# Optimization experiments

Hardware: AMD Instinct MI355X
Metric: run time of the kernel (lower is better)

Reference implementation:

```python
import jax, jax.numpy as jnp
import numpy as np

EPS = 1e-5

def layernorm(x, g, b):
    mu = jnp.mean(x, axis=-1, keepdims=True)
    var = jnp.var(x, axis=-1, keepdims=True)
    return (x - mu) * jax.lax.rsqrt(var + EPS) * g + b

DIM = 1024; CTX = 1024; HEADS = 12; DHEAD = 64; INNER = HEADS * DHEAD
B = 4; F = 2048; J = 1024

def setup_inputs() -> dict:
    key = jax.random.key(0)
    ks = jax.random.split(key, 8)
    s = lambda d: 1.0 / np.sqrt(d)
    return {
        "x": jax.random.normal(ks[0], (B, F, DIM), jnp.float32),
        "tab_x": jax.random.normal(ks[1], (B, J, CTX), jnp.float32),
        "tab_g": jnp.ones((CTX,), jnp.float32), "tab_b": jnp.zeros((CTX,), jnp.float32),
        "vid_g": jnp.ones((DIM,), jnp.float32), "vid_b": jnp.zeros((DIM,), jnp.float32),
        "Wq": jax.random.normal(ks[2], (DIM, INNER), jnp.float32) * s(DIM),
        "Wk": jax.random.normal(ks[3], (CTX, INNER), jnp.float32) * s(CTX),
        "Wv": jax.random.normal(ks[4], (CTX, INNER), jnp.float32) * s(CTX),
        "q_g": jnp.ones((INNER,), jnp.float32), "q_b": jnp.zeros((INNER,), jnp.float32),
        "k_g": jnp.ones((INNER,), jnp.float32), "k_b": jnp.zeros((INNER,), jnp.float32),
        "Wo": jax.random.normal(ks[5], (INNER, DIM), jnp.float32) * s(INNER),
        "bo": jnp.zeros((DIM,), jnp.float32),
    }

def reference(x, tab_x, tab_g, tab_b, vid_g, vid_b, Wq, Wk, Wv, q_g, q_b, k_g, k_b, Wo, bo):
    scale = DHEAD ** -0.5
    kv_in = layernorm(tab_x, tab_g, tab_b)                      # [b,j,ctx]
    q = layernorm(layernorm(x, vid_g, vid_b) @ Wq, q_g, q_b)    # [b,f,inner]
    k = layernorm(kv_in @ Wk, k_g, k_b)                         # [b,j,inner]
    v = kv_in @ Wv                                              # [b,j,inner]
    split = lambda t: t.reshape(t.shape[0], t.shape[1], HEADS, DHEAD).transpose(0, 2, 1, 3)
    q, k, v = split(q) * scale, split(k), split(v)              # [b,h,*,d]
    sim = jnp.einsum('bhid,bhjd->bhij', q, k)
    attn = jax.nn.softmax(sim, axis=-1)
    out = jnp.einsum('bhij,bhjd->bhid', attn, v)                # [b,h,f,d]
    out = out.transpose(0, 2, 1, 3).reshape(x.shape[0], x.shape[1], INNER)
    return out @ Wo + bo
```

## Files before the change

### kernel.cpp

```cpp
#include <hip/hip_runtime.h>

typedef unsigned short u16;
typedef float  f32x4   __attribute__((ext_vector_type(4)));
typedef float  f32x16  __attribute__((ext_vector_type(16)));
typedef __bf16 bf16x8  __attribute__((ext_vector_type(8)));
typedef u16    u16x4   __attribute__((ext_vector_type(4)));

#define DEV __device__ __forceinline__

DEV u16 f2bf(float f) {
  union { float f; unsigned u; } x; x.f = f;
  unsigned r = x.u + 0x7fffu + ((x.u >> 16) & 1u);
  return (u16)(r >> 16);
}
DEV float bf2f(u16 b) { union { unsigned u; float f; } c; c.u = (unsigned)b << 16; return c.f; }

DEV unsigned cvtpk(float lo, float hi) {
  unsigned r;
  asm("v_cvt_pk_bf16_f32 %0, %1, %2" : "=v"(r) : "v"(lo), "v"(hi));
  return r;
}

DEV f32x4 mfma16(bf16x8 a, bf16x8 b, f32x4 c) {
  return __builtin_amdgcn_mfma_f32_16x16x32_bf16(a, b, c, 0, 0, 0);
}
DEV f32x16 mfma32(bf16x8 a, bf16x8 b, f32x16 c) {
  return __builtin_amdgcn_mfma_f32_32x32x16_bf16(a, b, c, 0, 0, 0);
}

DEV void gload16(const void* g, void* l) {
  __builtin_amdgcn_global_load_lds(
      (__attribute__((address_space(1))) void*)g,
      (__attribute__((address_space(3))) void*)l, 16, 0, 0);
}

template<typename LOADER>
DEV void ln_body(LOADER load, const float* __restrict__ g, const float* __restrict__ bta,
                 u16* __restrict__ yrow, int C, float outscale, float* red)
{
  const int tid = threadIdx.x;
  const int n4 = C >> 2;
  f32x4 v = {0.f, 0.f, 0.f, 0.f};
  if (tid < n4) v = load(tid);
  float s1 = v[0] + v[1] + v[2] + v[3];
  float s2 = v[0]*v[0] + v[1]*v[1] + v[2]*v[2] + v[3]*v[3];
#pragma unroll
  for (int o = 32; o > 0; o >>= 1) {
    s1 += __shfl_xor(s1, o, 64);
    s2 += __shfl_xor(s2, o, 64);
  }
  const int lane = tid & 63, wv = tid >> 6;
  if (lane == 0) { red[wv] = s1; red[4 + wv] = s2; }
  __syncthreads();
  s1 = red[0] + red[1] + red[2] + red[3];
  s2 = red[4] + red[5] + red[6] + red[7];
  const float mu = s1 / C;
  const float rs = rsqrtf(s2 / C - mu * mu + 1e-5f);
  if (tid < n4) {
    f32x4 gg = *(const f32x4*)(g + 4 * tid);
    f32x4 bb = *(const f32x4*)(bta + 4 * tid);
    u16x4 o4;
#pragma unroll
    for (int j = 0; j < 4; ++j)
      o4[j] = f2bf(((v[j] - mu) * rs * gg[j] + bb[j]) * outscale);
    *(u16x4*)(yrow + 4 * tid) = o4;
  }
}

__global__ __launch_bounds__(256)
void prep(const float* __restrict__ Wq, const float* __restrict__ Wk,
          const float* __restrict__ Wv, const float* __restrict__ Wo,
          u16* __restrict__ WqT, u16* __restrict__ WkvT, u16* __restrict__ WoT,
          const float* __restrict__ tabx, const float* __restrict__ tab_g,
          const float* __restrict__ tab_b,
          const float* __restrict__ x, const float* __restrict__ vid_g,
          const float* __restrict__ vid_b,
          u16* __restrict__ kvn, u16* __restrict__ xn)
{
  __shared__ float t[32][33];
  __shared__ float red[8];
  const int bid = blockIdx.x;
  const int tid = threadIdx.x;
  if (bid < 3840) {
    const float* src; u16* dst; int K, N, k0, n0;
    if (bid < 3072) {
      const int w = bid / 768, r = bid % 768;
      src = (w == 0) ? Wq : (w == 1) ? Wk : Wv;
      dst = (w == 0) ? WqT : (w == 1) ? WkvT : WkvT + (size_t)768 * 1024;
      K = 1024; N = 768; k0 = (r % 32) * 32; n0 = (r / 32) * 32;
    } else {
      const int r = bid - 3072;
      src = Wo; dst = WoT;
      K = 768; N = 1024; k0 = (r % 24) * 32; n0 = (r / 24) * 32;
    }
    const int tx = tid & 31, ty = tid >> 5;
#pragma unroll
    for (int i = ty; i < 32; i += 8)
      t[i][tx] = src[(size_t)(k0 + i) * N + n0 + tx];
    __syncthreads();
#pragma unroll
    for (int i = ty; i < 32; i += 8)
      dst[(size_t)(n0 + i) * K + k0 + tx] = f2bf(t[tx][i]);
  } else {
    const int r = bid - 3840;
    const float* xr; const float *g, *bb; u16* y;
    if (r < 4096) { xr = tabx + (size_t)r * 1024; g = tab_g; bb = tab_b;
                    y = kvn + (size_t)r * 1024; }
    else { const int rr = r - 4096; xr = x + (size_t)rr * 1024; g = vid_g;
           bb = vid_b; y = xn + (size_t)rr * 1024; }
    ln_body([&](int i) { return *(const f32x4*)(xr + 4 * i); }, g, bb, y, 1024, 1.0f, red);
  }
}

__global__ __launch_bounds__(256)
void gemm_qkv(const u16* __restrict__ xn, const u16* __restrict__ kvn,
              const u16* __restrict__ WqT, const u16* __restrict__ WkvT,
              u16* __restrict__ q_pre, u16* __restrict__ k_pre, u16* __restrict__ vb)
{
  __shared__ __align__(16) u16 As[2][64 * 64];
  __shared__ __align__(16) u16 Bs[2][128 * 64];
  const int bid = blockIdx.x;
  const int tid  = threadIdx.x;
  const int lane = tid & 63;
  const int wave = tid >> 6;
  const bool isq = bid >= 768;
  const u16* A; const u16* Bt; int bm, bn;
  if (!isq) { A = kvn;  Bt = WkvT; bm = (bid & 63) * 64;  bn = (bid >> 6) * 128; }
  else { const int r = bid - 768; A = xn; Bt = WqT; bm = (r & 127) * 64; bn = (r >> 7) * 128; }
  const int wm = (wave >> 1) * 32;
  const int wn = (wave & 1) * 64;
  const int fr = lane & 15;
  const int fk = (lane >> 4) * 8;

  f32x4 acc[2][4] = {};
  const char* gA0 = (const char*)(A  + (size_t)bm * 1024);
  const char* gB0 = (const char*)(Bt + (size_t)bn * 1024);
  const size_t rowpitch = 2048;

  auto stage = [&](int buf, int k0) {
#pragma unroll
    for (int c = 0; c < 2; ++c) {
      const int off = tid * 16 + c * 4096;
      gload16(gA0 + (size_t)(off >> 7) * rowpitch + 2 * k0 + (off & 127),
              (char*)&As[buf][0] + wave * 1024 + c * 4096);
    }
#pragma unroll
    for (int c = 0; c < 4; ++c) {
      const int off = tid * 16 + c * 4096;
      gload16(gB0 + (size_t)(off >> 7) * rowpitch + 2 * k0 + (off & 127),
              (char*)&Bs[buf][0] + wave * 1024 + c * 4096);
    }
  };

  stage(0, 0);
  __syncthreads();
  int cur = 0;
  for (int t = 0; t < 16; ++t) {
    if (t + 1 < 16) stage(cur ^ 1, (t + 1) * 64);
    bf16x8 af[2][2], bg[4][2];
#pragma unroll
    for (int m = 0; m < 2; ++m)
#pragma unroll
      for (int kk = 0; kk < 2; ++kk)
        af[m][kk] = *(const bf16x8*)&As[cur][(wm + m * 16 + fr) * 64 + kk * 32 + fk];
#pragma unroll
    for (int n = 0; n < 4; ++n)
#pragma unroll
      for (int kk = 0; kk < 2; ++kk)
        bg[n][kk] = *(const bf16x8*)&Bs[cur][(wn + n * 16 + fr) * 64 + kk * 32 + fk];
#pragma unroll
    for (int kk = 0; kk < 2; ++kk)
#pragma unroll
      for (int m = 0; m < 2; ++m)
#pragma unroll
        for (int n = 0; n < 4; ++n)
          acc[m][n] = mfma16(af[m][kk], bg[n][kk], acc[m][n]);
    if (t + 1 < 16) __syncthreads();
    cur ^= 1;
  }

  const int orow0 = bm + wm + 4 * (lane >> 4);
  const int ocol0 = bn + wn + fr;
#pragma unroll
  for (int m = 0; m < 2; ++m)
#pragma unroll
    for (int n = 0; n < 4; ++n)
#pragma unroll
      for (int r = 0; r < 4; ++r) {
        const int row = orow0 + m * 16 + r;
        const int col = ocol0 + n * 16;
        const u16 v = f2bf(acc[m][n][r]);
        if (isq) q_pre[(size_t)row * 768 + col] = v;
        else if (bn < 768) k_pre[(size_t)row * 768 + col] = v;
        else               vb[(size_t)row * 768 + (col - 768)] = v;
      }
}

__global__ __launch_bounds__(256)
void ln_tv(const u16* __restrict__ k_pre, const float* __restrict__ k_g,
           const float* __restrict__ k_b, u16* __restrict__ kb,
           const u16* __restrict__ q_pre, const float* __restrict__ q_g,
           const float* __restrict__ q_b, u16* __restrict__ qb,
           const u16* __restrict__ vb, u16* __restrict__ vT)
{
  __shared__ u16 t[64][65];
  __shared__ float red[8];
  const int bid = blockIdx.x;
  const int tid = threadIdx.x;
  if (bid < 12288) {
    const bool isk = bid < 4096;
    const int row = isk ? bid : bid - 4096;
    const u16* xr = (isk ? k_pre : q_pre) + (size_t)row * 768;
    u16* y = (isk ? kb : qb) + (size_t)row * 768;
    const float sc = isk ? 1.0f : 0.125f * 1.44269504089f;
    ln_body([&](int i) {
      const u16x4 raw = *(const u16x4*)(xr + 4 * i);
      f32x4 v; 
#pragma unroll
      for (int j = 0; j < 4; ++j) v[j] = bf2f(raw[j]);
      return v;
    }, isk ? k_g : q_g, isk ? k_b : q_b, y, 768, sc, red);
  } else {
    const int r2 = bid - 12288;
    const int bh = r2 % 48, b = bh / 12, h = bh - b * 12;
    const int j0 = (r2 / 48) * 64;
    const int tx = tid & 63, ty = tid >> 6;
#pragma unroll
    for (int i = ty; i < 64; i += 4)
      t[i][tx] = vb[(size_t)(b * 1024 + j0 + i) * 768 + h * 64 + tx];
    __syncthreads();
#pragma unroll
    for (int i = ty; i < 64; i += 4)
      vT[((size_t)bh * 64 + i) * 1024 + j0 + tx] = t[tx][i];
  }
}

__global__ __launch_bounds__(256, 3)
void attn4(const u16* __restrict__ q, const u16* __restrict__ k,
           const u16* __restrict__ vT, u16* __restrict__ att)
{
  __shared__ __align__(16) u16 Ks[2][64 * 64];
  __shared__ __align__(16) u16 Vs[2][64 * 64];
  __shared__ __align__(16) u16 osm[4][32][72];

  const int bh = blockIdx.x;
  const int b = bh / 12, h = bh - b * 12;
  const int tid = threadIdx.x, lane = tid & 63, wave = tid >> 6;
  const int lq  = lane & 31;
  const int hi5 = lane >> 5;
  const int qrow = blockIdx.y * 128 + wave * 32 + lq;

  const u16* qp = q + (size_t)(b * 2048 + qrow) * 768 + h * 64 + hi5 * 8;
  bf16x8 qf[4];
#pragma unroll
  for (int ds = 0; ds < 4; ++ds) qf[ds] = *(const bf16x8*)(qp + ds * 16);

  f32x16 ot0 = {}, ot1 = {};
  float m = -1e30f, l = 0.f;

  const char* kg = (const char*)k + (size_t)(b * 1024) * 1536 + h * 128;
  const char* vg = (const char*)vT + (size_t)bh * 64 * 2048;
  const int rsw0 = (lq & 7) << 4;

  auto stage = [&](int buf, int j0) {
#pragma unroll
    for (int c = 0; c < 2; ++c) {
      const int o   = tid * 16 + c * 4096;
      const int row = o >> 7;
      const int scol = (o & 127) ^ ((row & 7) << 4);
      gload16(kg + (size_t)(j0 + row) * 1536 + scol,
              (char*)&Ks[buf][0] + wave * 1024 + c * 4096);
      gload16(vg + (size_t)row * 2048 + j0 * 2 + scol,
              (char*)&Vs[buf][0] + wave * 1024 + c * 4096);
    }
  };

  stage(0, 0);
  __syncthreads();
  int cur = 0;
  for (int t = 0; t < 16; ++t) {
    const int j0 = t * 64;
    if (t + 1 < 16) stage(cur ^ 1, j0 + 64);
    f32x16 st0 = {}, st1 = {};
    __builtin_amdgcn_s_setprio(1);
#pragma unroll
    for (int ds = 0; ds < 4; ++ds) {
      const int cb = ds * 32 + hi5 * 16;
      const bf16x8 k0 = *(const bf16x8*)((const char*)&Ks[cur][0] + lq * 128 + (cb ^ rsw0));
      const bf16x8 k1 = *(const bf16x8*)((const char*)&Ks[cur][0] + (lq + 32) * 128 + (cb ^ rsw0));
      st0 = mfma32(k0, qf[ds], st0);
      st1 = mfma32(k1, qf[ds], st1);
    }
    __builtin_amdgcn_s_setprio(0);
    float ta0 = fmaxf(st0[0], st1[0]), ta1 = fmaxf(st0[1], st1[1]);
    float ta2 = fmaxf(st0[2], st1[2]), ta3 = fmaxf(st0[3], st1[3]);
#pragma unroll
    for (int r = 4; r < 16; r += 4) {
      ta0 = fmaxf(fmaxf(st0[r],     st1[r]),     ta0);
      ta1 = fmaxf(fmaxf(st0[r + 1], st1[r + 1]), ta1);
      ta2 = fmaxf(fmaxf(st0[r + 2], st1[r + 2]), ta2);
      ta3 = fmaxf(fmaxf(st0[r + 3], st1[r + 3]), ta3);
    }
    float tmax = fmaxf(fmaxf(fmaxf(ta0, ta1), ta2), ta3);
    tmax = fmaxf(tmax, __shfl_xor(tmax, 32, 64));
    if (!__all(tmax - m <= 11.5416f)) {
      const float mn = fmaxf(m, tmax);
      const float sc = exp2f(m - mn);
      l *= sc;
#pragma unroll
      for (int r = 0; r < 16; ++r) { ot0[r] *= sc; ot1[r] *= sc; }
      m = mn;
    }
    float sa0 = 0.f, sa1 = 0.f, sa2 = 0.f, sa3 = 0.f;
#pragma unroll
    for (int r = 0; r < 16; r += 4) {
      float p0 = exp2f(st0[r]     - m); st0[r]     = p0; sa0 += p0;
      float p1 = exp2f(st0[r + 1] - m); st0[r + 1] = p1; sa1 += p1;
      float p2 = exp2f(st0[r + 2] - m); st0[r + 2] = p2; sa2 += p2;
      float p3 = exp2f(st0[r + 3] - m); st0[r + 3] = p3; sa3 += p3;
    }
#pragma unroll
    for (int r = 0; r < 16; r += 4) {
      float p0 = exp2f(st1[r]     - m); st1[r]     = p0; sa0 += p0;
      float p1 = exp2f(st1[r + 1] - m); st1[r + 1] = p1; sa1 += p1;
      float p2 = exp2f(st1[r + 2] - m); st1[r + 2] = p2; sa2 += p2;
      float p3 = exp2f(st1[r + 3] - m); st1[r + 3] = p3; sa3 += p3;
    }
    float ts = (sa0 + sa1) + (sa2 + sa3);
    ts += __shfl_xor(ts, 32, 64);
    l += ts;
    __builtin_amdgcn_s_setprio(1);
#pragma unroll
    for (int s4 = 0; s4 < 4; ++s4) {
      const int u = (s4 & 1) * 8;
      float a0, a1, a2, a3, b0, b1, b2, b3;
      if (s4 < 2) {
        a0 = st0[u]; a1 = st0[u + 1]; a2 = st0[u + 2]; a3 = st0[u + 3];
        b0 = st0[u + 4]; b1 = st0[u + 5]; b2 = st0[u + 6]; b3 = st0[u + 7];
      } else {
        a0 = st1[u]; a1 = st1[u + 1]; a2 = st1[u + 2]; a3 = st1[u + 3];
        b0 = st1[u + 4]; b1 = st1[u + 5]; b2 = st1[u + 6]; b3 = st1[u + 7];
      }
      const unsigned L0 = cvtpk(a0, a1), L1 = cvtpk(a2, a3);
      const unsigned H0 = cvtpk(b0, b1), H1 = cvtpk(b2, b3);
      const auto w02 = __builtin_amdgcn_permlane32_swap(L0, H0, false, false);
      const auto w13 = __builtin_amdgcn_permlane32_swap(L1, H1, false, false);
      union BU { unsigned w[4]; bf16x8 v; } pu;
      pu.w[0] = w02[0]; pu.w[1] = w13[0]; pu.w[2] = w02[1]; pu.w[3] = w13[1];
      const int cb = s4 * 32 + hi5 * 16;
      const bf16x8 v0 = *(const bf16x8*)((const char*)&Vs[cur][0] + lq * 128 + (cb ^ rsw0));
      const bf16x8 v1 = *(const bf16x8*)((const char*)&Vs[cur][0] + (lq + 32) * 128 + (cb ^ rsw0));
      ot0 = mfma32(v0, pu.v, ot0);
      ot1 = mfma32(v1, pu.v, ot1);
    }
    __builtin_amdgcn_s_setprio(0);
    if (t + 1 < 16) __syncthreads();
    cur ^= 1;
  }
  const float inv = 1.0f / l;
#pragma unroll
  for (int r = 0; r < 16; ++r) {
    const int d0 = (r & 3) + 8 * (r >> 2) + 4 * hi5;
    osm[wave][lq][d0]      = f2bf(ot0[r] * inv);
    osm[wave][lq][32 + d0] = f2bf(ot1[r] * inv);
  }
  __syncthreads();
  const int col = (lane & 7) * 8;
#pragma unroll
  for (int pass = 0; pass < 4; ++pass) {
    const int row = pass * 8 + (lane >> 3);
    const bf16x8 vv = *(const bf16x8*)&osm[wave][row][col];
    const int qg = blockIdx.y * 128 + wave * 32 + row;
    *(bf16x8*)(att + (size_t)(b * 2048 + qg) * 768 + h * 64 + col) = vv;
  }
}

__global__ __launch_bounds__(256)
void gemm_o(const u16* __restrict__ A, const u16* __restrict__ Bt,
            float* __restrict__ Cp, const float* __restrict__ bias)
{
  __shared__ __align__(16) u16 As[2][64 * 64];
  __shared__ __align__(16) u16 Bs[2][128 * 64];
  const int tid  = threadIdx.x;
  const int lane = tid & 63;
  const int wave = tid >> 6;
  const int bm = blockIdx.x * 64;
  const int bn = blockIdx.y * 128;
  const int wm = (wave >> 1) * 32;
  const int wn = (wave & 1) * 64;
  const int fr = lane & 15;
  const int fk = (lane >> 4) * 8;

  f32x4 acc[2][4] = {};
  const char* gA0 = (const char*)(A  + (size_t)bm * 768);
  const char* gB0 = (const char*)(Bt + (size_t)bn * 768);
  const size_t rowpitch = 1536;

  auto stage = [&](int buf, int k0) {
#pragma unroll
    for (int c = 0; c < 2; ++c) {
      const int off = tid * 16 + c * 4096;
      gload16(gA0 + (size_t)(off >> 7) * rowpitch + 2 * k0 + (off & 127),
              (char*)&As[buf][0] + wave * 1024 + c * 4096);
    }
#pragma unroll
    for (int c = 0; c < 4; ++c) {
      const int off = tid * 16 + c * 4096;
      gload16(gB0 + (size_t)(off >> 7) * rowpitch + 2 * k0 + (off & 127),
              (char*)&Bs[buf][0] + wave * 1024 + c * 4096);
    }
  };

  stage(0, 0);
  __syncthreads();
  int cur = 0;
  for (int t = 0; t < 12; ++t) {
    if (t + 1 < 12) stage(cur ^ 1, (t + 1) * 64);
    bf16x8 af[2][2], bg[4][2];
#pragma unroll
    for (int m = 0; m < 2; ++m)
#pragma unroll
      for (int kk = 0; kk < 2; ++kk)
        af[m][kk] = *(const bf16x8*)&As[cur][(wm + m * 16 + fr) * 64 + kk * 32 + fk];
#pragma unroll
    for (int n = 0; n < 4; ++n)
#pragma unroll
      for (int kk = 0; kk < 2; ++kk)
        bg[n][kk] = *(const bf16x8*)&Bs[cur][(wn + n * 16 + fr) * 64 + kk * 32 + fk];
#pragma unroll
    for (int kk = 0; kk < 2; ++kk)
#pragma unroll
      for (int m = 0; m < 2; ++m)
#pragma unroll
        for (int n = 0; n < 4; ++n)
          acc[m][n] = mfma16(af[m][kk], bg[n][kk], acc[m][n]);
    if (t + 1 < 12) __syncthreads();
    cur ^= 1;
  }

  const int orow0 = bm + wm + 4 * (lane >> 4);
  const int ocol0 = bn + wn + fr;
#pragma unroll
  for (int m = 0; m < 2; ++m)
#pragma unroll
    for (int n = 0; n < 4; ++n)
#pragma unroll
      for (int r = 0; r < 4; ++r) {
        const int row = orow0 + m * 16 + r;
        const int col = ocol0 + n * 16;
        Cp[(size_t)row * 1024 + col] = acc[m][n][r] + bias[col];
      }
}

extern "C" void kernel_launch(void* const* d_in, const int* in_sizes, int n_in,
                              void* d_out, int out_size, void* d_ws, size_t ws_size,
                              hipStream_t stream)
{
  const float* x     = (const float*)d_in[0];
  const float* tabx  = (const float*)d_in[1];
  const float* tab_g = (const float*)d_in[2];
  const float* tab_b = (const float*)d_in[3];
  const float* vid_g = (const float*)d_in[4];
  const float* vid_b = (const float*)d_in[5];
  const float* Wq    = (const float*)d_in[6];
  const float* Wk    = (const float*)d_in[7];
  const float* Wv    = (const float*)d_in[8];
  const float* q_g   = (const float*)d_in[9];
  const float* q_b   = (const float*)d_in[10];
  const float* k_g   = (const float*)d_in[11];
  const float* k_b   = (const float*)d_in[12];
  const float* Wo    = (const float*)d_in[13];
  const float* bo    = (const float*)d_in[14];

  char* ws = (char*)d_ws;
  const size_t O_WQT  = 0;
  const size_t O_WKVT = O_WQT  + (size_t)768 * 1024 * 2;
  const size_t O_WOT  = O_WKVT + (size_t)1536 * 1024 * 2;
  const size_t O_XN   = O_WOT  + (size_t)1024 * 768 * 2;
  const size_t O_KVN  = O_XN   + (size_t)8192 * 1024 * 2;
  const size_t O_QPRE = O_KVN  + (size_t)4096 * 1024 * 2;
  const size_t O_KPRE = O_QPRE + (size_t)8192 * 768 * 2;
  const size_t O_QB   = O_KPRE + (size_t)4096 * 768 * 2;
  const size_t O_KB   = O_QB   + (size_t)8192 * 768 * 2;
  const size_t O_VB   = O_KB   + (size_t)4096 * 768 * 2;
  const size_t O_VT   = O_VB   + (size_t)4096 * 768 * 2;
  const size_t O_ATT  = O_QPRE;

  u16*   WqT   = (u16*)(ws + O_WQT);
  u16*   WkvT  = (u16*)(ws + O_WKVT);
  u16*   WoT   = (u16*)(ws + O_WOT);
  u16*   xn    = (u16*)(ws + O_XN);
  u16*   kvn   = (u16*)(ws + O_KVN);
  u16*   q_pre = (u16*)(ws + O_QPRE);
  u16*   k_pre = (u16*)(ws + O_KPRE);
  u16*   qb    = (u16*)(ws + O_QB);
  u16*   kb    = (u16*)(ws + O_KB);
  u16*   vb    = (u16*)(ws + O_VB);
  u16*   vT    = (u16*)(ws + O_VT);
  u16*   attb  = (u16*)(ws + O_ATT);

  prep<<<16128, 256, 0, stream>>>(Wq, Wk, Wv, Wo, WqT, WkvT, WoT,
                                  tabx, tab_g, tab_b, x, vid_g, vid_b, kvn, xn);
  gemm_qkv<<<1536, 256, 0, stream>>>(xn, kvn, WqT, WkvT, q_pre, k_pre, vb);
  ln_tv<<<13056, 256, 0, stream>>>(k_pre, k_g, k_b, kb, q_pre, q_g, q_b, qb, vb, vT);
  attn4<<<dim3(48, 16), 256, 0, stream>>>(qb, kb, vT, attb);
  gemm_o<<<dim3(128, 8), 256, 0, stream>>>(attb, WoT, (float*)d_out, bo);
}
```

Before: 156.9 us.

## Write V transposed from QKV GEMM and split attention keys across wave groups

```diff
diff --git a/kernel.cpp b/kernel.cpp
--- a/kernel.cpp
+++ b/kernel.cpp
@@ -115,7 +115,7 @@
 __global__ __launch_bounds__(256)
 void gemm_qkv(const u16* __restrict__ xn, const u16* __restrict__ kvn,
               const u16* __restrict__ WqT, const u16* __restrict__ WkvT,
-              u16* __restrict__ q_pre, u16* __restrict__ k_pre, u16* __restrict__ vb)
+              u16* __restrict__ q_pre, u16* __restrict__ k_pre, u16* __restrict__ vT)
 {
   __shared__ __align__(16) u16 As[2][64 * 64];
   __shared__ __align__(16) u16 Bs[2][128 * 64];
@@ -184,71 +184,62 @@
 #pragma unroll
   for (int m = 0; m < 2; ++m)
 #pragma unroll
-    for (int n = 0; n < 4; ++n)
-#pragma unroll
-      for (int r = 0; r < 4; ++r) {
-        const int row = orow0 + m * 16 + r;
-        const int col = ocol0 + n * 16;
-        const u16 v = f2bf(acc[m][n][r]);
-        if (isq) q_pre[(size_t)row * 768 + col] = v;
-        else if (bn < 768) k_pre[(size_t)row * 768 + col] = v;
-        else               vb[(size_t)row * 768 + (col - 768)] = v;
+    for (int n = 0; n < 4; ++n) {
+      const int row0 = orow0 + m * 16;
+      const int col  = ocol0 + n * 16;
+      if (isq) {
+#pragma unroll
+        for (int r = 0; r < 4; ++r)
+          q_pre[(size_t)(row0 + r) * 768 + col] = f2bf(acc[m][n][r]);
+      } else if (bn < 768) {
+#pragma unroll
+        for (int r = 0; r < 4; ++r)
+          k_pre[(size_t)(row0 + r) * 768 + col] = f2bf(acc[m][n][r]);
+      } else {
+        const int c2 = col - 768, hh = c2 >> 6, dd = c2 & 63;
+        const int bb2 = row0 >> 10, jj = row0 & 1023;
+        u16x4 o4;
+#pragma unroll
+        for (int r = 0; r < 4; ++r) o4[r] = f2bf(acc[m][n][r]);
+        *(u16x4*)(vT + ((size_t)(bb2 * 12 + hh) * 64 + dd) * 1024 + jj) = o4;
       }
+    }
 }
 
 __global__ __launch_bounds__(256)
-void ln_tv(const u16* __restrict__ k_pre, const float* __restrict__ k_g,
+void ln_qk(const u16* __restrict__ k_pre, const float* __restrict__ k_g,
            const float* __restrict__ k_b, u16* __restrict__ kb,
            const u16* __restrict__ q_pre, const float* __restrict__ q_g,
-           const float* __restrict__ q_b, u16* __restrict__ qb,
-           const u16* __restrict__ vb, u16* __restrict__ vT)
-{
-  __shared__ u16 t[64][65];
+           const float* __restrict__ q_b, u16* __restrict__ qb)
+{
   __shared__ float red[8];
   const int bid = blockIdx.x;
-  const int tid = threadIdx.x;
-  if (bid < 12288) {
-    const bool isk = bid < 4096;
-    const int row = isk ? bid : bid - 4096;
-    const u16* xr = (isk ? k_pre : q_pre) + (size_t)row * 768;
-    u16* y = (isk ? kb : qb) + (size_t)row * 768;
-    const float sc = isk ? 1.0f : 0.125f * 1.44269504089f;
-    ln_body([&](int i) {
-      const u16x4 raw = *(const u16x4*)(xr + 4 * i);
-      f32x4 v; 
-#pragma unroll
-      for (int j = 0; j < 4; ++j) v[j] = bf2f(raw[j]);
-      return v;
-    }, isk ? k_g : q_g, isk ? k_b : q_b, y, 768, sc, red);
-  } else {
-    const int r2 = bid - 12288;
-    const int bh = r2 % 48, b = bh / 12, h = bh - b * 12;
-    const int j0 = (r2 / 48) * 64;
-    const int tx = tid & 63, ty = tid >> 6;
-#pragma unroll
-    for (int i = ty; i < 64; i += 4)
-      t[i][tx] = vb[(size_t)(b * 1024 + j0 + i) * 768 + h * 64 + tx];
-    __syncthreads();
-#pragma unroll
-    for (int i = ty; i < 64; i += 4)
-      vT[((size_t)bh * 64 + i) * 1024 + j0 + tx] = t[tx][i];
-  }
-}
-
-__global__ __launch_bounds__(256, 3)
-void attn4(const u16* __restrict__ q, const u16* __restrict__ k,
+  const bool isk = bid < 4096;
+  const int row = isk ? bid : bid - 4096;
+  const u16* xr = (isk ? k_pre : q_pre) + (size_t)row * 768;
+  u16* y = (isk ? kb : qb) + (size_t)row * 768;
+  const float sc = isk ? 1.0f : 0.125f * 1.44269504089f;
+  ln_body([&](int i) {
+    const u16x4 raw = *(const u16x4*)(xr + 4 * i);
+    f32x4 v;
+#pragma unroll
+    for (int j = 0; j < 4; ++j) v[j] = bf2f(raw[j]);
+    return v;
+  }, isk ? k_g : q_g, isk ? k_b : q_b, y, 768, sc, red);
+}
+
+__global__ __launch_bounds__(512, 4)
+void attn5(const u16* __restrict__ q, const u16* __restrict__ k,
            const u16* __restrict__ vT, u16* __restrict__ att)
 {
-  __shared__ __align__(16) u16 Ks[2][64 * 64];
-  __shared__ __align__(16) u16 Vs[2][64 * 64];
-  __shared__ __align__(16) u16 osm[4][32][72];
+  __shared__ __align__(16) char smem[32768];
 
   const int bh = blockIdx.x;
   const int b = bh / 12, h = bh - b * 12;
   const int tid = threadIdx.x, lane = tid & 63, wave = tid >> 6;
-  const int lq  = lane & 31;
-  const int hi5 = lane >> 5;
-  const int qrow = blockIdx.y * 128 + wave * 32 + lq;
+  const int qsub = wave & 3, jgrp = wave >> 2;
+  const int lq = lane & 31, hi5 = lane >> 5;
+  const int qrow = blockIdx.y * 128 + qsub * 32 + lq;
 
   const u16* qp = q + (size_t)(b * 2048 + qrow) * 768 + h * 64 + hi5 * 8;
   bf16x8 qf[4];
@@ -262,32 +253,28 @@
   const char* vg = (const char*)vT + (size_t)bh * 64 * 2048;
   const int rsw0 = (lq & 7) << 4;
 
-  auto stage = [&](int buf, int j0) {
+  char* Kbuf = smem + jgrp * 8192;
+  char* Vbuf = smem + 16384 + jgrp * 8192;
+  const int gtid = tid & 255;
+
+  for (int t = 0; t < 8; ++t) {
+    const int j0 = jgrp * 512 + t * 64;
 #pragma unroll
     for (int c = 0; c < 2; ++c) {
-      const int o   = tid * 16 + c * 4096;
+      const int o   = gtid * 16 + c * 4096;
       const int row = o >> 7;
       const int scol = (o & 127) ^ ((row & 7) << 4);
-      gload16(kg + (size_t)(j0 + row) * 1536 + scol,
-              (char*)&Ks[buf][0] + wave * 1024 + c * 4096);
-      gload16(vg + (size_t)row * 2048 + j0 * 2 + scol,
-              (char*)&Vs[buf][0] + wave * 1024 + c * 4096);
-    }
-  };
-
-  stage(0, 0);
-  __syncthreads();
-  int cur = 0;
-  for (int t = 0; t < 16; ++t) {
-    const int j0 = t * 64;
-    if (t + 1 < 16) stage(cur ^ 1, j0 + 64);
+      gload16(kg + (size_t)(j0 + row) * 1536 + scol, Kbuf + qsub * 1024 + c * 4096);
+      gload16(vg + (size_t)row * 2048 + (size_t)j0 * 2 + scol, Vbuf + qsub * 1024 + c * 4096);
+    }
+    __syncthreads();
     f32x16 st0 = {}, st1 = {};
     __builtin_amdgcn_s_setprio(1);
 #pragma unroll
     for (int ds = 0; ds < 4; ++ds) {
       const int cb = ds * 32 + hi5 * 16;
-      const bf16x8 k0 = *(const bf16x8*)((const char*)&Ks[cur][0] + lq * 128 + (cb ^ rsw0));
-      const bf16x8 k1 = *(const bf16x8*)((const char*)&Ks[cur][0] + (lq + 32) * 128 + (cb ^ rsw0));
+      const bf16x8 k0 = *(const bf16x8*)(Kbuf + lq * 128 + (cb ^ rsw0));
+      const bf16x8 k1 = *(const bf16x8*)(Kbuf + (lq + 32) * 128 + (cb ^ rsw0));
       st0 = mfma32(k0, qf[ds], st0);
       st1 = mfma32(k1, qf[ds], st1);
     }
@@ -348,30 +335,63 @@
       union BU { unsigned w[4]; bf16x8 v; } pu;
       pu.w[0] = w02[0]; pu.w[1] = w13[0]; pu.w[2] = w02[1]; pu.w[3] = w13[1];
       const int cb = s4 * 32 + hi5 * 16;
-      const bf16x8 v0 = *(const bf16x8*)((const char*)&Vs[cur][0] + lq * 128 + (cb ^ rsw0));
-      const bf16x8 v1 = *(const bf16x8*)((const char*)&Vs[cur][0] + (lq + 32) * 128 + (cb ^ rsw0));
+      const bf16x8 v0 = *(const bf16x8*)(Vbuf + lq * 128 + (cb ^ rsw0));
+      const bf16x8 v1 = *(const bf16x8*)(Vbuf + (lq + 32) * 128 + (cb ^ rsw0));
       ot0 = mfma32(v0, pu.v, ot0);
       ot1 = mfma32(v1, pu.v, ot1);
     }
     __builtin_amdgcn_s_setprio(0);
-    if (t + 1 < 16) __syncthreads();
-    cur ^= 1;
-  }
-  const float inv = 1.0f / l;
-#pragma unroll
-  for (int r = 0; r < 16; ++r) {
-    const int d0 = (r & 3) + 8 * (r >> 2) + 4 * hi5;
-    osm[wave][lq][d0]      = f2bf(ot0[r] * inv);
-    osm[wave][lq][32 + d0] = f2bf(ot1[r] * inv);
-  }
-  __syncthreads();
-  const int col = (lane & 7) * 8;
-#pragma unroll
-  for (int pass = 0; pass < 4; ++pass) {
-    const int row = pass * 8 + (lane >> 3);
-    const bf16x8 vv = *(const bf16x8*)&osm[wave][row][col];
-    const int qg = blockIdx.y * 128 + wave * 32 + row;
-    *(bf16x8*)(att + (size_t)(b * 2048 + qg) * 768 + h * 64 + col) = vv;
+    __syncthreads();
+  }
+
+  float* mb = (float*)smem;
+  float* lb = mb + 256;
+  float* ob = lb + 256;
+  const int mi = qsub * 64 + lane;
+  if (jgrp) {
+    mb[mi] = m; lb[mi] = l;
+#pragma unroll
+    for (int r = 0; r < 16; ++r) ob[mi * 16 + r] = ot0[r];
+  }
+  __syncthreads();
+  float sA = 1.f, sB = 0.f;
+  if (!jgrp) {
+    const float mB = mb[mi], lB = lb[mi];
+    const float mm = fmaxf(m, mB);
+    sA = exp2f(m - mm); sB = exp2f(mB - mm);
+    l = l * sA + lB * sB;
+#pragma unroll
+    for (int r = 0; r < 16; ++r) ot0[r] = ot0[r] * sA + ob[mi * 16 + r] * sB;
+  }
+  __syncthreads();
+  if (jgrp) {
+#pragma unroll
+    for (int r = 0; r < 16; ++r) ob[mi * 16 + r] = ot1[r];
+  }
+  __syncthreads();
+  if (!jgrp) {
+#pragma unroll
+    for (int r = 0; r < 16; ++r) ot1[r] = ot1[r] * sA + ob[mi * 16 + r] * sB;
+  }
+  __syncthreads();
+  if (!jgrp) {
+    u16 (*osm)[72] = (u16(*)[72])smem + qsub * 32;
+    const float inv = 1.0f / l;
+#pragma unroll
+    for (int r = 0; r < 16; ++r) {
+      const int d0 = (r & 3) + 8 * (r >> 2) + 4 * hi5;
+      osm[lq][d0]      = f2bf(ot0[r] * inv);
+      osm[lq][32 + d0] = f2bf(ot1[r] * inv);
+    }
+    asm volatile("s_waitcnt lgkmcnt(0)" ::: "memory");
+    const int col = (lane & 7) * 8;
+#pragma unroll
+    for (int pass = 0; pass < 4; ++pass) {
+      const int row = pass * 8 + (lane >> 3);
+      const bf16x8 vv = *(const bf16x8*)&osm[row][col];
+      const int qg = blockIdx.y * 128 + qsub * 32 + row;
+      *(bf16x8*)(att + (size_t)(b * 2048 + qg) * 768 + h * 64 + col) = vv;
+    }
   }
 }
 
@@ -482,8 +502,7 @@
   const size_t O_KPRE = O_QPRE + (size_t)8192 * 768 * 2;
   const size_t O_QB   = O_KPRE + (size_t)4096 * 768 * 2;
   const size_t O_KB   = O_QB   + (size_t)8192 * 768 * 2;
-  const size_t O_VB   = O_KB   + (size_t)4096 * 768 * 2;
-  const size_t O_VT   = O_VB   + (size_t)4096 * 768 * 2;
+  const size_t O_VT   = O_KB   + (size_t)4096 * 768 * 2;
   const size_t O_ATT  = O_QPRE;
 
   u16*   WqT   = (u16*)(ws + O_WQT);
@@ -495,14 +514,13 @@
   u16*   k_pre = (u16*)(ws + O_KPRE);
   u16*   qb    = (u16*)(ws + O_QB);
   u16*   kb    = (u16*)(ws + O_KB);
-  u16*   vb    = (u16*)(ws + O_VB);
   u16*   vT    = (u16*)(ws + O_VT);
   u16*   attb  = (u16*)(ws + O_ATT);
 
   prep<<<16128, 256, 0, stream>>>(Wq, Wk, Wv, Wo, WqT, WkvT, WoT,
                                   tabx, tab_g, tab_b, x, vid_g, vid_b, kvn, xn);
-  gemm_qkv<<<1536, 256, 0, stream>>>(xn, kvn, WqT, WkvT, q_pre, k_pre, vb);
-  ln_tv<<<13056, 256, 0, stream>>>(k_pre, k_g, k_b, kb, q_pre, q_g, q_b, qb, vb, vT);
-  attn4<<<dim3(48, 16), 256, 0, stream>>>(qb, kb, vT, attb);
+  gemm_qkv<<<1536, 256, 0, stream>>>(xn, kvn, WqT, WkvT, q_pre, k_pre, vT);
+  ln_qk<<<12288, 256, 0, stream>>>(k_pre, k_g, k_b, kb, q_pre, q_g, q_b, qb);
+  attn5<<<dim3(48, 16), 512, 0, stream>>>(qb, kb, vT, attb);
   gemm_o<<<dim3(128, 8), 256, 0, stream>>>(attb, WoT, (float*)d_out, bo);
 }
```

New measurement: 157.1 us. No clear change (+0.1%).
